# Kernel optimization log

Measured on AMD Instinct MI355X. Metric: run time of the kernel, lower is better.

The kernel has to match this reference:

```python
import jax, jax.numpy as jnp
import numpy as np

B, C, N, M = 8, 128, 2048, 512

def setup_inputs() -> dict:
    key = jax.random.key(0)
    k1, k2, k3, k4 = jax.random.split(key, 4)
    scale = 1.0 / np.sqrt(C)
    x = jax.random.normal(k1, (B, C, N), dtype=jnp.float32)
    # conv1d with kernel size 1 and no bias == channel-mixing matmul, weight [C_out, C_in]
    Wq = jax.random.normal(k2, (C, C), dtype=jnp.float32) * scale
    Wk = jax.random.normal(k3, (C, C), dtype=jnp.float32) * scale
    Wv = jax.random.normal(k4, (C, C), dtype=jnp.float32) * scale
    return {"x": x, "Wq": Wq, "Wk": Wk, "Wv": Wv, "npts_ds": M}

def reference(x, Wq, Wk, Wv, npts_ds):
    # q,k,v: [B,C,N] via 1x1 conv == einsum over input channels
    q = jnp.einsum('oc,bcn->bon', Wq, x)
    k = jnp.einsum('oc,bcn->bon', Wk, x)
    v = jnp.einsum('oc,bcn->bon', Wv, x)
    # energy: [B,N,N] = q^T k (contract channel dim)
    energy = jnp.einsum('bcn,bcm->bnm', q, k)
    scale_factor = jnp.sqrt(jnp.asarray(q.shape[-2], dtype=energy.dtype))  # sqrt(C)
    attention = jax.nn.softmax(energy / scale_factor, axis=-1)  # [B,N,N]
    selection = jnp.sum(attention, axis=-2)  # [B,N] column sums
    _, idx = jax.lax.top_k(selection, npts_ds)  # [B,M]
    # gather selected attention rows: [B,M,N]
    scores = jnp.take_along_axis(attention, idx[:, :, None], axis=1)
    # weighted sum of values: [B,M,C]
    out = jnp.einsum('bmn,bcn->bcm', scores, v)  # [B,C,M]
    return out
```

## Files before the change

### kernel.cpp

```cpp
#include <hip/hip_runtime.h>
#include <math.h>

namespace {
constexpr int B = 8, C = 128, N = 2048, M = 512;
constexpr int NSPLIT = 8;
constexpr int MBLK = N / 128;
constexpr float INV_SQRT_C = 0.08838834764831845f;
}

typedef __attribute__((ext_vector_type(8))) short short8;
typedef __attribute__((ext_vector_type(16))) float f32x16;
typedef unsigned short ushort_t;
typedef unsigned int u32;

__device__ inline ushort_t f2bf(float f) {
  union { float f; u32 u; } a; a.f = f;
  u32 r = a.u + 0x7fffu + ((a.u >> 16) & 1u);
  return (ushort_t)(r >> 16);
}
__device__ inline float bf2f(ushort_t h) {
  union { u32 u; float f; } a; a.u = ((u32)h) << 16; return a.f;
}

__global__ __launch_bounds__(256) void qkv_kernel(
    const float* __restrict__ x, const float* __restrict__ Wq,
    const float* __restrict__ Wk, const float* __restrict__ Wv,
    ushort_t* __restrict__ split, float* __restrict__ v) {
  const size_t TERM = (size_t)B * N * C;
  int kc = blockIdx.x;
  int o0 = kc * 8;
  int n = blockIdx.y * 256 + threadIdx.x;
  int b = blockIdx.z;
  const float* xb = x + (size_t)b * C * N + n;
  float aq[8] = {}, ak[8] = {}, av[8] = {};
  #pragma unroll 4
  for (int c = 0; c < C; ++c) {
    float xv = xb[(size_t)c * N];
    #pragma unroll
    for (int j = 0; j < 8; ++j) {
      aq[j] = fmaf(Wq[(o0 + j) * C + c], xv, aq[j]);
      ak[j] = fmaf(Wk[(o0 + j) * C + c], xv, ak[j]);
      av[j] = fmaf(Wv[(o0 + j) * C + c], xv, av[j]);
    }
  }
  #pragma unroll
  for (int j = 0; j < 8; ++j)
    v[((size_t)b * C + o0 + j) * N + n] = av[j];
  size_t rowoff = ((size_t)b * 16 + kc) * (size_t)N * 8 + (size_t)n * 8;
  #pragma unroll
  for (int tt = 0; tt < 3; ++tt) {
    short8 qv, kv;
    #pragma unroll
    for (int j = 0; j < 8; ++j) {
      ushort_t h = f2bf(aq[j]); qv[j] = (short)h; aq[j] -= bf2f(h);
      h = f2bf(ak[j]);          kv[j] = (short)h; ak[j] -= bf2f(h);
    }
    *(short8*)&split[tt * TERM + rowoff]       = qv;
    *(short8*)&split[(3 + tt) * TERM + rowoff] = kv;
  }
}

__global__ __launch_bounds__(256) void energy_kernel(
    const ushort_t* __restrict__ split,
    float* __restrict__ Ae, float* __restrict__ rowpart) {
  __shared__ float red[128][64];
  __shared__ float red2[128][2];
  const size_t TERM = (size_t)B * N * C;
  const size_t ROW8 = (size_t)N * 8;
  int t = threadIdx.x;
  int lane = t & 63, w = t >> 6;
  int wn = w & 1, wm = w >> 1;
  int lin = blockIdx.y * 16 + blockIdx.x;
  int st = lin >> 4, wi = lin & 15;
  int mb = (st & 3) * 4 + (wi & 3);
  int nb = (st >> 2) * 4 + (wi >> 2);
  int m0 = mb * 128, n0 = nb * 128, b = blockIdx.z;
  int lr = lane & 31, lq = lane >> 5;
  size_t kbase = ((size_t)b * 16 + lq) * ROW8;
  const ushort_t* Abase = split + kbase + (size_t)(n0 + wn * 64 + lr) * 8;
  const ushort_t* Bbase = split + 3 * TERM + kbase + (size_t)(m0 + wm * 64 + lr) * 8;
  f32x16 acc[2][2] = {};
  #pragma unroll
  for (int s = 0; s < 8; ++s) {
    size_t so = (size_t)s * 2 * ROW8;
    short8 aT[3][2], bT[3][2];
    #pragma unroll
    for (int tt = 0; tt < 3; ++tt)
      #pragma unroll
      for (int i = 0; i < 2; ++i) {
        aT[tt][i] = *(const short8*)(Abase + tt * TERM + so + i * 256);
        bT[tt][i] = *(const short8*)(Bbase + tt * TERM + so + i * 256);
      }
    #pragma unroll
    for (int mt = 0; mt < 2; ++mt)
      #pragma unroll
      for (int nt = 0; nt < 2; ++nt) {
        acc[mt][nt] = __builtin_amdgcn_mfma_f32_32x32x16_bf16(aT[0][mt], bT[0][nt], acc[mt][nt], 0, 0, 0);
        acc[mt][nt] = __builtin_amdgcn_mfma_f32_32x32x16_bf16(aT[1][mt], bT[0][nt], acc[mt][nt], 0, 0, 0);
        acc[mt][nt] = __builtin_amdgcn_mfma_f32_32x32x16_bf16(aT[0][mt], bT[1][nt], acc[mt][nt], 0, 0, 0);
        acc[mt][nt] = __builtin_amdgcn_mfma_f32_32x32x16_bf16(aT[2][mt], bT[0][nt], acc[mt][nt], 0, 0, 0);
        acc[mt][nt] = __builtin_amdgcn_mfma_f32_32x32x16_bf16(aT[1][mt], bT[1][nt], acc[mt][nt], 0, 0, 0);
        acc[mt][nt] = __builtin_amdgcn_mfma_f32_32x32x16_bf16(aT[0][mt], bT[2][nt], acc[mt][nt], 0, 0, 0);
      }
  }
  int lc = lr;
  #pragma unroll
  for (int mt = 0; mt < 2; ++mt) {
    #pragma unroll
    for (int reg = 0; reg < 16; ++reg) {
      int row = (reg & 3) + 8 * (reg >> 2) + 4 * lq;
      int rloc = wn * 64 + mt * 32 + row;
      float e0 = expf(acc[mt][0][reg] * INV_SQRT_C);
      float e1 = expf(acc[mt][1][reg] * INV_SQRT_C);
      float* pA = Ae + ((size_t)b * N + n0 + rloc) * N + m0 + wm * 64 + lc;
      pA[0] = e0; pA[32] = e1;
      red[rloc][wm * 32 + lc] = e0 + e1;
    }
  }
  __syncthreads();
  {
    int row = t >> 1, h = t & 1;
    float ssum = 0.f;
    #pragma unroll
    for (int j0 = 0; j0 < 32; ++j0) {
      int j = (j0 + (t & 31)) & 31;
      ssum += red[row][h * 32 + j];
    }
    red2[row][h] = ssum;
  }
  __syncthreads();
  if (t < 128)
    rowpart[(size_t)mb * (B * N) + b * N + n0 + t] = red2[t][0] + red2[t][1];
}

__global__ __launch_bounds__(256) void rowred_kernel(
    const float* __restrict__ rowpart, float* __restrict__ invr) {
  int i = blockIdx.x * 256 + threadIdx.x;
  float s = 0.f;
  #pragma unroll
  for (int mb = 0; mb < MBLK; ++mb)
    s += rowpart[(size_t)mb * (B * N) + i];
  invr[i] = 1.0f / s;
}

__global__ __launch_bounds__(256) void colsum_kernel(
    const float* __restrict__ Ae, const float* __restrict__ invr,
    float* __restrict__ selpart) {
  int m = blockIdx.x * 256 + threadIdx.x;
  int nch = blockIdx.y, b = blockIdx.z;
  const float* Ab = Ae + (size_t)b * N * N;
  const float* ib = invr + b * N;
  float acc = 0.f;
  int n0 = nch * (N / 8);
  for (int n = n0; n < n0 + N / 8; ++n)
    acc = fmaf(Ab[(size_t)n * N + m], ib[n], acc);
  selpart[(size_t)nch * (B * N) + b * N + m] = acc;
}

__global__ __launch_bounds__(256) void selred_kernel(
    const float* __restrict__ selpart, float* __restrict__ sel) {
  int i = blockIdx.x * 256 + threadIdx.x;
  float s = 0.f;
  #pragma unroll
  for (int nch = 0; nch < 8; ++nch)
    s += selpart[(size_t)nch * (B * N) + i];
  sel[i] = s;
}

__global__ __launch_bounds__(256) void topk_kernel(
    const float* __restrict__ sel, int* __restrict__ idx) {
  __shared__ float s[N];
  __shared__ int rsum[64][4];
  int b = blockIdx.y;
  int t = threadIdx.x;
  for (int i = t; i < N; i += 256) s[i] = sel[b * N + i];
  __syncthreads();
  int i = blockIdx.x * 64 + (t & 63);
  int jc = t >> 6;
  float val = s[i];
  int r = 0;
  for (int j = jc * 512; j < jc * 512 + 512; ++j) {
    float sj = s[j];
    r += (sj > val || (sj == val && j < i)) ? 1 : 0;
  }
  rsum[t & 63][jc] = r;
  __syncthreads();
  if (t < 64) {
    int rank = rsum[t][0] + rsum[t][1] + rsum[t][2] + rsum[t][3];
    if (rank < M) idx[b * M + rank] = blockIdx.x * 64 + t;
  }
}

__global__ __launch_bounds__(256) void out_kernel(
    const float* __restrict__ Ae, const float* __restrict__ invr,
    const float* __restrict__ v, const int* __restrict__ idx,
    float* __restrict__ part) {
  __shared__ float vt[32][133];
  __shared__ float wt[32][133];
  __shared__ int ridx[128];
  __shared__ float rinv[128];
  int t = threadIdx.x;
  int m0 = blockIdx.x * 128;
  int ns = blockIdx.y;
  int b = blockIdx.z;
  if (t < 128) {
    int r = idx[b * M + m0 + t];
    ridx[t] = r;
    rinv[t] = invr[b * N + r];
  }
  __syncthreads();
  int tc = t & 15, tm = t >> 4;
  float acc[8][8] = {};
  const float* vb = v + (size_t)b * C * N;
  const float* Ab = Ae + (size_t)b * N * N;
  int nbeg = ns * (N / NSPLIT);
  for (int nb = nbeg; nb < nbeg + N / NSPLIT; nb += 32) {
    __syncthreads();
    #pragma unroll
    for (int it = 0; it < 16; ++it) {
      int ii = it * 256 + t;
      int c = ii >> 5, nn = ii & 31;
      vt[nn][c] = vb[(size_t)c * N + nb + nn];
    }
    #pragma unroll
    for (int it = 0; it < 16; ++it) {
      int ii = it * 256 + t;
      int mm = ii >> 5, nn = ii & 31;
      wt[nn][mm] = Ab[(size_t)ridx[mm] * N + nb + nn] * rinv[mm];
    }
    __syncthreads();
    #pragma unroll
    for (int nn = 0; nn < 32; ++nn) {
      float4 a0 = *(const float4*)&vt[nn][tc * 8];
      float4 a1 = *(const float4*)&vt[nn][tc * 8 + 4];
      float4 b0 = *(const float4*)&wt[nn][tm * 8];
      float4 b1 = *(const float4*)&wt[nn][tm * 8 + 4];
      float av[8] = {a0.x, a0.y, a0.z, a0.w, a1.x, a1.y, a1.z, a1.w};
      float wv[8] = {b0.x, b0.y, b0.z, b0.w, b1.x, b1.y, b1.z, b1.w};
      #pragma unroll
      for (int ci = 0; ci < 8; ++ci)
        #pragma unroll
        for (int mj = 0; mj < 8; ++mj)
          acc[ci][mj] = fmaf(av[ci], wv[mj], acc[ci][mj]);
    }
  }
  float* pb = part + ((size_t)ns * B + b) * C * M;
  #pragma unroll
  for (int ci = 0; ci < 8; ++ci) {
    size_t rowoff = (size_t)(tc * 8 + ci) * M + m0 + tm * 8;
    *(float4*)&pb[rowoff] = make_float4(acc[ci][0], acc[ci][1], acc[ci][2], acc[ci][3]);
    *(float4*)&pb[rowoff + 4] = make_float4(acc[ci][4], acc[ci][5], acc[ci][6], acc[ci][7]);
  }
}

__global__ __launch_bounds__(256) void reduce_kernel(
    const float* __restrict__ part, float* __restrict__ out) {
  int i = blockIdx.x * 256 + threadIdx.x;
  float a = 0.f;
  #pragma unroll
  for (int ns = 0; ns < NSPLIT; ++ns)
    a += part[(size_t)ns * (B * C * M) + i];
  out[i] = a;
}

extern "C" void kernel_launch(void* const* d_in, const int* in_sizes, int n_in,
                              void* d_out, int out_size, void* d_ws, size_t ws_size,
                              hipStream_t stream) {
  const float* x  = (const float*)d_in[0];
  const float* Wq = (const float*)d_in[1];
  const float* Wk = (const float*)d_in[2];
  const float* Wv = (const float*)d_in[3];
  float* out = (float*)d_out;

  const size_t TSZ = (size_t)B * N * C;
  ushort_t* split = (ushort_t*)d_ws;
  float* v       = (float*)(split + 6 * TSZ);
  float* Ae      = v + (size_t)B * C * N;
  float* rowpart = Ae + (size_t)B * N * N;
  float* invr    = rowpart + (size_t)MBLK * B * N;
  float* selpart = invr + (size_t)B * N;
  float* sel     = selpart + (size_t)8 * B * N;
  int*   idx     = (int*)(sel + (size_t)B * N);
  float* part    = (float*)split;

  qkv_kernel<<<dim3(16, N / 256, B), 256, 0, stream>>>(x, Wq, Wk, Wv, split, v);
  energy_kernel<<<dim3(N / 128, N / 128, B), 256, 0, stream>>>(split, Ae, rowpart);
  rowred_kernel<<<dim3(B * N / 256), 256, 0, stream>>>(rowpart, invr);
  colsum_kernel<<<dim3(N / 256, 8, B), 256, 0, stream>>>(Ae, invr, selpart);
  selred_kernel<<<dim3(B * N / 256), 256, 0, stream>>>(selpart, sel);
  topk_kernel<<<dim3(N / 64, B), 256, 0, stream>>>(sel, idx);
  out_kernel<<<dim3(M / 128, NSPLIT, B), 256, 0, stream>>>(Ae, invr, v, idx, part);
  reduce_kernel<<<dim3(B * C * M / 256), 256, 0, stream>>>(part, out);
}
```

Baseline: 276.9 us.

## Use bf16 MFMA in out kernel, shuffle row sums, fuse selection reduce into topk

The output GEMM switches from an fp32 FMA register tile to bf16 MFMA 32x32x16, converting gathered attention rows and values to bf16 in shared memory. The energy kernel replaces its shared-memory row-sum reduction and two barriers with wavefront shuffles, writing 32 partial slots per row. The colsum split is doubled to 16 chunks, and the separate selection-reduce kernel is folded into the topk kernel's load. Rounding attention weights to bf16 lowers output precision and could perturb results, and each topk block now re-sums the 16 partials.

Measured after the change: 304.2 us. +9.8%, slower.

```diff
diff --git a/kernel.cpp b/kernel.cpp
--- a/kernel.cpp
+++ b/kernel.cpp
@@ -4,7 +4,8 @@
 namespace {
 constexpr int B = 8, C = 128, N = 2048, M = 512;
 constexpr int NSPLIT = 8;
-constexpr int MBLK = N / 128;
+constexpr int RSLOT = 32;
+constexpr int CSLOT = 16;
 constexpr float INV_SQRT_C = 0.08838834764831845f;
 }
 
@@ -63,8 +64,6 @@
 __global__ __launch_bounds__(256) void energy_kernel(
     const ushort_t* __restrict__ split,
     float* __restrict__ Ae, float* __restrict__ rowpart) {
-  __shared__ float red[128][64];
-  __shared__ float red2[128][2];
   const size_t TERM = (size_t)B * N * C;
   const size_t ROW8 = (size_t)N * 8;
   int t = threadIdx.x;
@@ -103,7 +102,7 @@
         acc[mt][nt] = __builtin_amdgcn_mfma_f32_32x32x16_bf16(aT[0][mt], bT[2][nt], acc[mt][nt], 0, 0, 0);
       }
   }
-  int lc = lr;
+  float* rp = rowpart + (size_t)(mb * 2 + wm) * (B * N) + b * N;
   #pragma unroll
   for (int mt = 0; mt < 2; ++mt) {
     #pragma unroll
@@ -112,25 +111,17 @@
       int rloc = wn * 64 + mt * 32 + row;
       float e0 = expf(acc[mt][0][reg] * INV_SQRT_C);
       float e1 = expf(acc[mt][1][reg] * INV_SQRT_C);
-      float* pA = Ae + ((size_t)b * N + n0 + rloc) * N + m0 + wm * 64 + lc;
+      float* pA = Ae + ((size_t)b * N + n0 + rloc) * N + m0 + wm * 64 + lr;
       pA[0] = e0; pA[32] = e1;
-      red[rloc][wm * 32 + lc] = e0 + e1;
-    }
-  }
-  __syncthreads();
-  {
-    int row = t >> 1, h = t & 1;
-    float ssum = 0.f;
-    #pragma unroll
-    for (int j0 = 0; j0 < 32; ++j0) {
-      int j = (j0 + (t & 31)) & 31;
-      ssum += red[row][h * 32 + j];
-    }
-    red2[row][h] = ssum;
-  }
-  __syncthreads();
-  if (t < 128)
-    rowpart[(size_t)mb * (B * N) + b * N + n0 + t] = red2[t][0] + red2[t][1];
+      float val = e0 + e1;
+      val += __shfl_xor(val, 1);
+      val += __shfl_xor(val, 2);
+      val += __shfl_xor(val, 4);
+      val += __shfl_xor(val, 8);
+      val += __shfl_xor(val, 16);
+      if (lr == 0) rp[n0 + rloc] = val;
+    }
+  }
 }
 
 __global__ __launch_bounds__(256) void rowred_kernel(
@@ -138,8 +129,8 @@
   int i = blockIdx.x * 256 + threadIdx.x;
   float s = 0.f;
   #pragma unroll
-  for (int mb = 0; mb < MBLK; ++mb)
-    s += rowpart[(size_t)mb * (B * N) + i];
+  for (int sl = 0; sl < RSLOT; ++sl)
+    s += rowpart[(size_t)sl * (B * N) + i];
   invr[i] = 1.0f / s;
 }
 
@@ -151,29 +142,26 @@
   const float* Ab = Ae + (size_t)b * N * N;
   const float* ib = invr + b * N;
   float acc = 0.f;
-  int n0 = nch * (N / 8);
-  for (int n = n0; n < n0 + N / 8; ++n)
+  int n0 = nch * (N / CSLOT);
+  #pragma unroll 4
+  for (int n = n0; n < n0 + N / CSLOT; ++n)
     acc = fmaf(Ab[(size_t)n * N + m], ib[n], acc);
   selpart[(size_t)nch * (B * N) + b * N + m] = acc;
 }
 
-__global__ __launch_bounds__(256) void selred_kernel(
-    const float* __restrict__ selpart, float* __restrict__ sel) {
-  int i = blockIdx.x * 256 + threadIdx.x;
-  float s = 0.f;
-  #pragma unroll
-  for (int nch = 0; nch < 8; ++nch)
-    s += selpart[(size_t)nch * (B * N) + i];
-  sel[i] = s;
-}
-
 __global__ __launch_bounds__(256) void topk_kernel(
-    const float* __restrict__ sel, int* __restrict__ idx) {
+    const float* __restrict__ selpart, int* __restrict__ idx) {
   __shared__ float s[N];
   __shared__ int rsum[64][4];
   int b = blockIdx.y;
   int t = threadIdx.x;
-  for (int i = t; i < N; i += 256) s[i] = sel[b * N + i];
+  for (int i = t; i < N; i += 256) {
+    float v_ = 0.f;
+    #pragma unroll
+    for (int nch = 0; nch < CSLOT; ++nch)
+      v_ += selpart[(size_t)nch * (B * N) + b * N + i];
+    s[i] = v_;
+  }
   __syncthreads();
   int i = blockIdx.x * 64 + (t & 63);
   int jc = t >> 6;
@@ -195,8 +183,8 @@
     const float* __restrict__ Ae, const float* __restrict__ invr,
     const float* __restrict__ v, const int* __restrict__ idx,
     float* __restrict__ part) {
-  __shared__ float vt[32][133];
-  __shared__ float wt[32][133];
+  __shared__ ushort_t sc[128][72];
+  __shared__ ushort_t vt[128][72];
   __shared__ int ridx[128];
   __shared__ float rinv[128];
   int t = threadIdx.x;
@@ -209,47 +197,52 @@
     rinv[t] = invr[b * N + r];
   }
   __syncthreads();
-  int tc = t & 15, tm = t >> 4;
-  float acc[8][8] = {};
-  const float* vb = v + (size_t)b * C * N;
-  const float* Ab = Ae + (size_t)b * N * N;
+  int lane = t & 63, w = t >> 6;
+  int wc = w & 1, wm = w >> 1;
+  int lr = lane & 31, lq = lane >> 5;
+  f32x16 acc[2][2] = {};
   int nbeg = ns * (N / NSPLIT);
-  for (int nb = nbeg; nb < nbeg + N / NSPLIT; nb += 32) {
+  for (int kb = 0; kb < N / NSPLIT; kb += 64) {
     __syncthreads();
     #pragma unroll
-    for (int it = 0; it < 16; ++it) {
+    for (int it = 0; it < 32; ++it) {
       int ii = it * 256 + t;
-      int c = ii >> 5, nn = ii & 31;
-      vt[nn][c] = vb[(size_t)c * N + nb + nn];
-    }
-    #pragma unroll
-    for (int it = 0; it < 16; ++it) {
+      int r = ii >> 6, cn = ii & 63;
+      float sv = Ae[((size_t)b * N + ridx[r]) * N + nbeg + kb + cn] * rinv[r];
+      sc[r][cn] = f2bf(sv);
+    }
+    #pragma unroll
+    for (int it = 0; it < 32; ++it) {
       int ii = it * 256 + t;
-      int mm = ii >> 5, nn = ii & 31;
-      wt[nn][mm] = Ab[(size_t)ridx[mm] * N + nb + nn] * rinv[mm];
+      int r = ii >> 6, cn = ii & 63;
+      vt[r][cn] = f2bf(v[((size_t)b * C + r) * N + nbeg + kb + cn]);
     }
     __syncthreads();
     #pragma unroll
-    for (int nn = 0; nn < 32; ++nn) {
-      float4 a0 = *(const float4*)&vt[nn][tc * 8];
-      float4 a1 = *(const float4*)&vt[nn][tc * 8 + 4];
-      float4 b0 = *(const float4*)&wt[nn][tm * 8];
-      float4 b1 = *(const float4*)&wt[nn][tm * 8 + 4];
-      float av[8] = {a0.x, a0.y, a0.z, a0.w, a1.x, a1.y, a1.z, a1.w};
-      float wv[8] = {b0.x, b0.y, b0.z, b0.w, b1.x, b1.y, b1.z, b1.w};
-      #pragma unroll
-      for (int ci = 0; ci < 8; ++ci)
+    for (int ks = 0; ks < 4; ++ks) {
+      short8 af[2], bf_[2];
+      #pragma unroll
+      for (int i = 0; i < 2; ++i) {
+        af[i]  = *(const short8*)&vt[wc * 64 + i * 32 + lr][ks * 16 + lq * 8];
+        bf_[i] = *(const short8*)&sc[wm * 64 + i * 32 + lr][ks * 16 + lq * 8];
+      }
+      #pragma unroll
+      for (int ct = 0; ct < 2; ++ct)
         #pragma unroll
-        for (int mj = 0; mj < 8; ++mj)
-          acc[ci][mj] = fmaf(av[ci], wv[mj], acc[ci][mj]);
+        for (int mt = 0; mt < 2; ++mt)
+          acc[ct][mt] = __builtin_amdgcn_mfma_f32_32x32x16_bf16(af[ct], bf_[mt], acc[ct][mt], 0, 0, 0);
     }
   }
   float* pb = part + ((size_t)ns * B + b) * C * M;
   #pragma unroll
-  for (int ci = 0; ci < 8; ++ci) {
-    size_t rowoff = (size_t)(tc * 8 + ci) * M + m0 + tm * 8;
-    *(float4*)&pb[rowoff] = make_float4(acc[ci][0], acc[ci][1], acc[ci][2], acc[ci][3]);
-    *(float4*)&pb[rowoff + 4] = make_float4(acc[ci][4], acc[ci][5], acc[ci][6], acc[ci][7]);
+  for (int ct = 0; ct < 2; ++ct) {
+    #pragma unroll
+    for (int reg = 0; reg < 16; ++reg) {
+      int crow = wc * 64 + ct * 32 + (reg & 3) + 8 * (reg >> 2) + 4 * lq;
+      #pragma unroll
+      for (int mt = 0; mt < 2; ++mt)
+        pb[(size_t)crow * M + m0 + wm * 64 + mt * 32 + lr] = acc[ct][mt][reg];
+    }
   }
 }
 
@@ -277,18 +270,16 @@
   float* v       = (float*)(split + 6 * TSZ);
   float* Ae      = v + (size_t)B * C * N;
   float* rowpart = Ae + (size_t)B * N * N;
-  float* invr    = rowpart + (size_t)MBLK * B * N;
+  float* invr    = rowpart + (size_t)RSLOT * B * N;
   float* selpart = invr + (size_t)B * N;
-  float* sel     = selpart + (size_t)8 * B * N;
-  int*   idx     = (int*)(sel + (size_t)B * N);
+  int*   idx     = (int*)(selpart + (size_t)CSLOT * B * N);
   float* part    = (float*)split;
 
   qkv_kernel<<<dim3(16, N / 256, B), 256, 0, stream>>>(x, Wq, Wk, Wv, split, v);
   energy_kernel<<<dim3(N / 128, N / 128, B), 256, 0, stream>>>(split, Ae, rowpart);
   rowred_kernel<<<dim3(B * N / 256), 256, 0, stream>>>(rowpart, invr);
-  colsum_kernel<<<dim3(N / 256, 8, B), 256, 0, stream>>>(Ae, invr, selpart);
-  selred_kernel<<<dim3(B * N / 256), 256, 0, stream>>>(selpart, sel);
-  topk_kernel<<<dim3(N / 64, B), 256, 0, stream>>>(sel, idx);
+  colsum_kernel<<<dim3(N / 256, CSLOT, B), 256, 0, stream>>>(Ae, invr, selpart);
+  topk_kernel<<<dim3(N / 64, B), 256, 0, stream>>>(selpart, idx);
   out_kernel<<<dim3(M / 128, NSPLIT, B), 256, 0, stream>>>(Ae, invr, v, idx, part);
   reduce_kernel<<<dim3(B * C * M / 256), 256, 0, stream>>>(part, out);
 }
```
